# Kernel tuning notes

Measured on AMD Instinct MI355X. Metric: run time of the kernel, lower is better.

## Reference

```python
import jax, jax.numpy as jnp
import numpy as np

N_BISECT_ITERS = 50  # entmax library default


def entmax_bisect(X, alpha, n_iter=N_BISECT_ITERS):
    """alpha-entmax over last axis via bisection (Peters & Martins 2019).
    Solves for tau s.t. sum(max((alpha-1)X - tau, 0)^(1/(alpha-1))) = 1."""
    am1 = alpha - 1.0
    inv = 1.0 / am1
    Xa = X * am1
    max_val = jnp.max(Xa, axis=-1, keepdims=True)
    d = X.shape[-1]
    tau_lo = max_val - 1.0                                   # _gp(1, alpha) = 1
    tau_hi = max_val - jnp.asarray(1.0 / d, X.dtype) ** am1  # _gp(1/d, alpha)

    def pfun(tau):
        return jnp.maximum(Xa - tau, 0.0) ** inv

    f_lo = jnp.sum(pfun(tau_lo), axis=-1, keepdims=True) - 1.0

    def body(i, carry):
        tau_lo, dm = carry
        dm = dm * 0.5
        tau_m = tau_lo + dm
        f_m = jnp.sum(pfun(tau_m), axis=-1, keepdims=True) - 1.0
        tau_lo = jnp.where(f_m * f_lo >= 0, tau_m, tau_lo)
        return (tau_lo, dm)

    tau_lo, _ = jax.lax.fori_loop(0, n_iter, body, (tau_lo, tau_hi - tau_lo))
    p = pfun(tau_lo)
    return p / jnp.sum(p, axis=-1, keepdims=True)  # ensure_sum_one


def setup_inputs() -> dict:
    master = jax.random.key(0)
    kq, kk, kv = jax.random.split(master, 3)
    B, H, S, D = 4, 16, 2048, 64
    return {
        "query": jax.random.normal(kq, (B, H, S, D), jnp.float32),
        "key": jax.random.normal(kk, (B, H, S, D), jnp.float32),
        "value": jax.random.normal(kv, (B, H, S, D), jnp.float32),
        "alpha": jnp.float32(1.5),  # canonical entmax-1.5
    }


def reference(query, key, value, alpha):
    D = query.shape[-1]
    scale = 1.0 / jnp.sqrt(jnp.asarray(D, query.dtype))
    scores = jnp.einsum('bhqd,bhkd->bhqk', query, key) * scale  # [B,H,S,S]
    p_attn = entmax_bisect(scores, alpha)
    out = jnp.einsum('bhqk,bhkd->bhqd', p_attn, value)
    return (out, p_attn)
```

## Files before the change

kernel.cpp:

```cpp
#include <hip/hip_runtime.h>
#include <math.h>

#define S_LEN 2048
#define HD    64
#define QT    16
#define NT    1024
#define NW    16
#define NTIL  8
#define CAP   512
#define NITER 28
#define NEWT  10

typedef short s8v __attribute__((ext_vector_type(8)));
typedef float f4v __attribute__((ext_vector_type(4)));

template <bool B> struct BoolT { static constexpr bool value = B; };

__device__ __forceinline__ float wave_sum(float v) {
#pragma unroll
    for (int off = 32; off >= 1; off >>= 1)
        v += __shfl_xor(v, off, 64);
    return v;
}

__device__ __forceinline__ float group16_max(float v) {
#pragma unroll
    for (int off = 8; off >= 1; off >>= 1)
        v = fmaxf(v, __shfl_xor(v, off, 64));
    return v;
}

__device__ __forceinline__ unsigned f2bf2(float lo, float hi) {
    unsigned a = __float_as_uint(lo), b = __float_as_uint(hi);
    a += 0x7FFFu + ((a >> 16) & 1u);
    b += 0x7FFFu + ((b >> 16) & 1u);
    return (a >> 16) | (b & 0xFFFF0000u);
}

__device__ __forceinline__ unsigned short f2bf1(float x) {
    unsigned a = __float_as_uint(x);
    a += 0x7FFFu + ((a >> 16) & 1u);
    return (unsigned short)(a >> 16);
}

__device__ __forceinline__ s8v pack_bf8(const float4& x, const float4& y, float sc) {
    union { s8v s; unsigned u[4]; } f;
    f.u[0] = f2bf2(x.x * sc, x.y * sc);
    f.u[1] = f2bf2(x.z * sc, x.w * sc);
    f.u[2] = f2bf2(y.x * sc, y.y * sc);
    f.u[3] = f2bf2(y.z * sc, y.w * sc);
    return f.s;
}

template <bool INV2>
__device__ __forceinline__ float pfun_t(float t, float inv) {
    float u = fmaxf(t, 0.0f);
    return INV2 ? u * u : powf(u, inv);
}

template <int NR>
__device__ __forceinline__ void newton_reg(const float* cvrow, int ncp, int lane,
                                           float tau0, float& tau_out, float& isum_out) {
    float c[NR];
#pragma unroll
    for (int j = 0; j < NR; ++j) {
        int i = lane + 64 * j;
        c[j] = (i < ncp) ? cvrow[i] : -3.0e38f;
    }
    float tau = tau0;
#pragma unroll
    for (int it = 0; it < NEWT; ++it) {
        float s1 = 0.0f, s2 = 0.0f;
#pragma unroll
        for (int j = 0; j < NR; ++j) {
            float u = fmaxf(c[j] - tau, 0.0f);
            s1 += u;
            s2 = fmaf(u, u, s2);
        }
#pragma unroll
        for (int off = 32; off >= 1; off >>= 1) {
            s1 += __shfl_xor(s1, off, 64);
            s2 += __shfl_xor(s2, off, 64);
        }
        tau += (s2 - 1.0f) * 0.5f * __builtin_amdgcn_rcpf(fmaxf(s1, 1e-30f));
    }
    float s = 0.0f;
#pragma unroll
    for (int j = 0; j < NR; ++j) {
        float u = fmaxf(c[j] - tau, 0.0f);
        s = fmaf(u, u, s);
    }
    s = wave_sum(s);
    tau_out = tau;
    isum_out = 1.0f / s;
}

template <int NR, bool INV2>
__device__ __forceinline__ void bisect_reg(const float* cvrow, int ncp, int lane,
                                           float tau_lo0, float tau_hi, float inv,
                                           float& tau_out, float& isum_out) {
    float c[NR];
#pragma unroll
    for (int j = 0; j < NR; ++j) {
        int i = lane + 64 * j;
        c[j] = (i < ncp) ? cvrow[i] : -3.0e38f;
    }
    float tau = tau_lo0;
    float s0 = 0.0f;
#pragma unroll
    for (int j = 0; j < NR; ++j) s0 += pfun_t<INV2>(c[j] - tau, inv);
    const float f_lo = wave_sum(s0) - 1.0f;
    float dm = tau_hi - tau_lo0;
    for (int it = 0; it < NITER; ++it) {
        dm *= 0.5f;
        float tm = tau + dm;
        float s = 0.0f;
#pragma unroll
        for (int j = 0; j < NR; ++j) s += pfun_t<INV2>(c[j] - tm, inv);
        float fm = wave_sum(s) - 1.0f;
        if (fm * f_lo >= 0.0f) tau = tm;
    }
    float s = 0.0f;
#pragma unroll
    for (int j = 0; j < NR; ++j) s += pfun_t<INV2>(c[j] - tau, inv);
    float ssum = wave_sum(s);
    tau_out = tau;
    isum_out = 1.0f / ssum;
}

__global__ __launch_bounds__(256)
void pack_kv(const float* __restrict__ Kp, const float* __restrict__ Vp,
             s8v* __restrict__ Kb, s8v* __restrict__ Vb, int nK) {
    int idx = blockIdx.x * 256 + threadIdx.x;
    if (idx < nK) {
        const int lane = idx & 63, frag = (idx >> 6) & 1, tile = (idx >> 7) & 127, bh = idx >> 14;
        const int l16 = lane & 15, quad = lane >> 4;
        const float* src = Kp + ((size_t)(bh * S_LEN + tile * 16 + l16)) * HD + frag * 32 + quad * 8;
        float4 a = *(const float4*)src;
        float4 b = *(const float4*)(src + 4);
        Kb[idx] = pack_bf8(a, b, 1.0f);
    } else {
        int v = idx - nK;
        const int lane = v & 63, dt = (v >> 6) & 3, ktg = (v >> 8) & 63, bh = v >> 14;
        const int l16 = lane & 15, quad = lane >> 4;
        const float* src = Vp + ((size_t)(bh * S_LEN + ktg * 32 + quad * 8)) * HD + dt * 16 + l16;
        float w[8];
#pragma unroll
        for (int j = 0; j < 8; ++j) w[j] = src[(size_t)j * HD];
        float4 a = {w[0], w[1], w[2], w[3]};
        float4 b = {w[4], w[5], w[6], w[7]};
        Vb[v] = pack_bf8(a, b, 1.0f);
    }
}

template <bool PREK, bool DPV>
__global__ __launch_bounds__(NT)
void entmax_attn(const float* __restrict__ Qp, const float* __restrict__ Kp,
                 const float* __restrict__ Vp, const float* __restrict__ alphap,
                 float* __restrict__ outp, float* __restrict__ pattn,
                 const s8v* __restrict__ Kbf, const s8v* __restrict__ Vbf) {
    constexpr int SM_BIG = DPV ? (NW * QT * 68 * 4)
                               : (QT * CAP * 4 + QT * CAP * 2);
    __shared__ __align__(16) char smem[SM_BIG];
    float          (*candv)[CAP] = (float(*)[CAP])smem;
    unsigned short (*candi)[CAP] = (unsigned short(*)[CAP])(smem + QT * CAP * 4);

    __shared__ int   ncnt[QT];
    __shared__ float rmaxw[QT][NW];
    __shared__ float rmxf[QT];
    __shared__ float taus[QT];
    __shared__ float isums[QT];
    __shared__ float redw[NW];

    const int tid   = threadIdx.x;
    const int wv    = tid >> 6;
    const int lane  = tid & 63;
    const int quad  = lane >> 4;
    const int l16   = lane & 15;
    const int bh    = blockIdx.y;
    const int q0    = blockIdx.x * QT;
    const int wcol0 = wv * (NTIL * 16);

    const float alpha = alphap[0];
    const float am1   = alpha - 1.0f;
    const float inv   = 1.0f / am1;
    const bool  inv2  = (inv == 2.0f);
    const float xscale = (1.0f / sqrtf((float)HD)) * am1;
    const float gp_d   = powf(1.0f / (float)S_LEN, am1);

    if (tid < QT) ncnt[tid] = 0;

    const float* vbase = Vp + (size_t)bh * S_LEN * HD;

    s8v qa0, qa1;
    {
        const float* qp = Qp + ((size_t)bh * S_LEN + q0 + l16) * HD + quad * 8;
        float4 x0 = *(const float4*)qp;
        float4 x1 = *(const float4*)(qp + 4);
        float4 y0 = *(const float4*)(qp + 32);
        float4 y1 = *(const float4*)(qp + 36);
        qa0 = pack_bf8(x0, x1, xscale);
        qa1 = pack_bf8(y0, y1, xscale);
    }

    f4v xa[NTIL];
    if constexpr (PREK) {
        const s8v* kf = Kbf + ((size_t)bh * (S_LEN / 16) + (wcol0 >> 4)) * 2 * 64 + lane;
#pragma unroll
        for (int t = 0; t < NTIL; ++t) {
            s8v kb0 = kf[(2 * t    ) * 64];
            s8v kb1 = kf[(2 * t + 1) * 64];
            f4v acc = {0.0f, 0.0f, 0.0f, 0.0f};
            acc = __builtin_amdgcn_mfma_f32_16x16x32_bf16(qa0, kb0, acc, 0, 0, 0);
            acc = __builtin_amdgcn_mfma_f32_16x16x32_bf16(qa1, kb1, acc, 0, 0, 0);
            xa[t] = acc;
        }
    } else {
        const float* kbase = Kp + (size_t)bh * S_LEN * HD;
#pragma unroll
        for (int t = 0; t < NTIL; ++t) {
            const float* kp = kbase + ((size_t)(wcol0 + t * 16 + l16)) * HD + quad * 8;
            float4 k0 = *(const float4*)kp;
            float4 k1 = *(const float4*)(kp + 4);
            s8v kb0 = pack_bf8(k0, k1, 1.0f);
            f4v acc = {0.0f, 0.0f, 0.0f, 0.0f};
            acc = __builtin_amdgcn_mfma_f32_16x16x32_bf16(qa0, kb0, acc, 0, 0, 0);
            float4 k2 = *(const float4*)(kp + 32);
            float4 k3 = *(const float4*)(kp + 36);
            s8v kb1 = pack_bf8(k2, k3, 1.0f);
            acc = __builtin_amdgcn_mfma_f32_16x16x32_bf16(qa1, kb1, acc, 0, 0, 0);
            xa[t] = acc;
        }
    }

#pragma unroll
    for (int g = 0; g < 4; ++g) {
        float pm = xa[0][g];
#pragma unroll
        for (int t = 1; t < NTIL; ++t) pm = fmaxf(pm, xa[t][g]);
        pm = group16_max(pm);
        if (l16 == 0) rmaxw[quad * 4 + g][wv] = pm;
    }
    __syncthreads();
    if (tid < QT) {
        float m = rmaxw[tid][0];
#pragma unroll
        for (int w = 1; w < NW; ++w) m = fmaxf(m, rmaxw[tid][w]);
        rmxf[tid] = m;
    }
    __syncthreads();

    float tl0g[4];
#pragma unroll
    for (int g = 0; g < 4; ++g) tl0g[g] = rmxf[quad * 4 + g] - 1.0f;

#pragma unroll
    for (int t = 0; t < NTIL; ++t) {
#pragma unroll
        for (int g = 0; g < 4; ++g) {
            const float v = xa[t][g];
            const int row = quad * 4 + g;
            const bool pred = (v > tl0g[g]);
            unsigned long long m = __ballot(pred);
            unsigned gm16 = (unsigned)((m >> (quad * 16)) & 0xFFFFull);
            int base = 0;
            if (l16 == 0) {
                int cnt = __popc(gm16);
                if (cnt) base = atomicAdd(&ncnt[row], cnt);
            }
            base = __shfl(base, quad * 16, 64);
            if (pred) {
                int pos = base + __popc(gm16 & ((1u << l16) - 1u));
                if (pos < CAP) {
                    candv[row][pos] = v;
                    if constexpr (!DPV) candi[row][pos] = (unsigned short)(wcol0 + t * 16 + l16);
                }
            }
        }
    }
    __syncthreads();

    auto tail = [&](auto inv2c) {
        constexpr bool INV2 = decltype(inv2c)::value;

        {
            const int row = wv;
            const int nc = ncnt[row];
            if (nc <= CAP) {
                const int ncp = (nc + 7) & ~7;
                for (int i = nc + lane; i < ncp; i += 64) {
                    candv[row][i] = -3.0e38f;
                    if constexpr (!DPV) candi[row][i] = 0;
                }
                const float mx  = rmxf[row];
                const float tl0 = mx - 1.0f;
                const float th  = mx - gp_d;
                float tau, isum;
                if constexpr (INV2) {
                    if (ncp <= 256) newton_reg<4>(&candv[row][0], ncp, lane, tl0, tau, isum);
                    else            newton_reg<8>(&candv[row][0], ncp, lane, tl0, tau, isum);
                } else {
                    if (ncp <= 256) bisect_reg<4, INV2>(&candv[row][0], ncp, lane, tl0, th, inv, tau, isum);
                    else            bisect_reg<8, INV2>(&candv[row][0], ncp, lane, tl0, th, inv, tau, isum);
                }
                if (lane == 0) { taus[row] = tau; isums[row] = isum; }
            }
        }

#pragma unroll 1
        for (int r = 0; r < QT; ++r) {
            if (ncnt[r] > CAP) {
                const float mx = rmxf[r];
                const int g = r & 3;
                const bool mine = (quad == (r >> 2));
                float tau = mx - 1.0f;
                float s0 = 0.0f;
                if (mine) {
#pragma unroll
                    for (int t = 0; t < NTIL; ++t) s0 += pfun_t<INV2>(xa[t][g] - tau, inv);
                }
                s0 = wave_sum(s0);
                if (lane == 0) redw[wv] = s0;
                __syncthreads();
                float f_lo = -1.0f;
                for (int w = 0; w < NW; ++w) f_lo += redw[w];
                __syncthreads();
                float dm = (mx - gp_d) - tau;
                for (int it = 0; it < NITER; ++it) {
                    dm *= 0.5f;
                    float tm = tau + dm;
                    float s = 0.0f;
                    if (mine) {
#pragma unroll
                        for (int t = 0; t < NTIL; ++t) s += pfun_t<INV2>(xa[t][g] - tm, inv);
                    }
                    s = wave_sum(s);
                    if (lane == 0) redw[wv] = s;
                    __syncthreads();
                    float fm = -1.0f;
                    for (int w = 0; w < NW; ++w) fm += redw[w];
                    __syncthreads();
                    if (fm * f_lo >= 0.0f) tau = tm;
                }
                float s = 0.0f;
                if (mine) {
#pragma unroll
                    for (int t = 0; t < NTIL; ++t) s += pfun_t<INV2>(xa[t][g] - tau, inv);
                }
                s = wave_sum(s);
                if (lane == 0) redw[wv] = s;
                __syncthreads();
                float ssum = 0.0f;
                for (int w = 0; w < NW; ++w) ssum += redw[w];
                __syncthreads();
                if (tid == 0) { taus[r] = tau; isums[r] = 1.0f / ssum; }
            }
        }
        __syncthreads();

        if constexpr (DPV) {
            unsigned short* pwf = (unsigned short*)smem + wv * 2048;
            const size_t prow_base = ((size_t)bh * S_LEN + q0) * S_LEN;
#pragma unroll
            for (int g = 0; g < 4; ++g) {
                const int row = quad * 4 + g;
                const float tau  = taus[row];
                const float isum = isums[row];
                float* prow = pattn + prow_base + (size_t)row * S_LEN + wcol0 + l16;
#pragma unroll
                for (int t = 0; t < NTIL; ++t) {
                    float uu = fmaxf(xa[t][g] - tau, 0.0f);
                    float p2 = uu * uu;
                    prow[t * 16] = p2 * isum;
                    const int col   = t * 16 + l16;
                    const int slot  = ((col >> 3) ^ row) & 15;
                    pwf[row * 128 + slot * 8 + (col & 7)] = f2bf1(p2);
                }
            }
            s8v afrag[4];
#pragma unroll
            for (int kt = 0; kt < 4; ++kt) {
                const int slot = ((kt * 4 + quad) ^ l16) & 15;
                afrag[kt] = *(const s8v*)&pwf[l16 * 128 + slot * 8];
            }
            const s8v* vf = Vbf + ((size_t)bh * (S_LEN / 32) + (wcol0 >> 5)) * 4 * 64 + lane;
            f4v oacc[4];
#pragma unroll
            for (int dt = 0; dt < 4; ++dt) oacc[dt] = (f4v){0.0f, 0.0f, 0.0f, 0.0f};
#pragma unroll
            for (int kt = 0; kt < 4; ++kt) {
#pragma unroll
                for (int dt = 0; dt < 4; ++dt) {
                    s8v b = vf[(kt * 4 + dt) * 64];
                    oacc[dt] = __builtin_amdgcn_mfma_f32_16x16x32_bf16(afrag[kt], b, oacc[dt], 0, 0, 0);
                }
            }
            __syncthreads();
            float* part = (float*)smem;
#pragma unroll
            for (int dt = 0; dt < 4; ++dt) {
#pragma unroll
                for (int g = 0; g < 4; ++g) {
                    part[wv * (QT * 68) + (quad * 4 + g) * 68 + dt * 16 + l16] = oacc[dt][g];
                }
            }
            __syncthreads();
            float s = 0.0f;
#pragma unroll
            for (int w = 0; w < NW; ++w) s += part[w * (QT * 68) + wv * 68 + lane];
            outp[((size_t)bh * S_LEN + q0 + wv) * HD + lane] = s * isums[wv];
        } else {
            const size_t prow_base = ((size_t)bh * S_LEN + q0) * S_LEN;
#pragma unroll
            for (int g = 0; g < 4; ++g) {
                const int row = quad * 4 + g;
                const float tau  = taus[row];
                const float isum = isums[row];
                float* prow = pattn + prow_base + (size_t)row * S_LEN + wcol0 + l16;
#pragma unroll
                for (int t = 0; t < NTIL; ++t) {
                    prow[t * 16] = pfun_t<INV2>(xa[t][g] - tau, inv) * isum;
                }
            }
            __threadfence_block();
            __syncthreads();

            const int row  = wv;
            const int qrow = q0 + row;
            const int nc   = ncnt[row];
            const float tau  = taus[row];
            const float isum = isums[row];
            float oacc = 0.0f;
            if (nc <= CAP) {
                const int ncp = (nc + 7) & ~7;
                for (int i = lane; i < ncp; i += 64)
                    candv[row][i] = pfun_t<INV2>(candv[row][i] - tau, inv);
                float oacc1 = 0.0f;
                for (int i = 0; i < ncp; i += 8) {
#pragma unroll
                    for (int u = 0; u < 8; u += 2) {
                        oacc  = fmaf(candv[row][i + u],
                                     vbase[(size_t)candi[row][i + u] * HD + lane], oacc);
                        oacc1 = fmaf(candv[row][i + u + 1],
                                     vbase[(size_t)candi[row][i + u + 1] * HD + lane], oacc1);
                    }
                }
                oacc = (oacc + oacc1) * isum;
            } else {
                const float* prow = pattn + ((size_t)bh * S_LEN + qrow) * S_LEN;
                for (int k = 0; k < S_LEN; ++k)
                    oacc = fmaf(prow[k], vbase[(size_t)k * HD + lane], oacc);
            }
            outp[((size_t)bh * S_LEN + qrow) * HD + lane] = oacc;
        }
    };

    if (inv2) tail(BoolT<true>{});
    else      tail(BoolT<false>{});
}

extern "C" void kernel_launch(void* const* d_in, const int* in_sizes, int n_in,
                              void* d_out, int out_size, void* d_ws, size_t ws_size,
                              hipStream_t stream) {
    const float* Q = (const float*)d_in[0];
    const float* K = (const float*)d_in[1];
    const float* V = (const float*)d_in[2];
    const float* A = (const float*)d_in[3];
    float* out = (float*)d_out;
    const int BH = in_sizes[0] / (S_LEN * HD);
    float* p = out + (size_t)BH * S_LEN * HD;
    dim3 grid(S_LEN / QT, BH);

    const size_t kb_bytes = (size_t)BH * S_LEN * HD * sizeof(short);
    const int nK = BH * (S_LEN / 16) * 2 * 64;
    const int nV = BH * (S_LEN / 32) * 4 * 64;

    if (d_ws != nullptr && ws_size >= 2 * kb_bytes) {
        s8v* Kb = (s8v*)d_ws;
        s8v* Vb = (s8v*)((char*)d_ws + kb_bytes);
        pack_kv<<<dim3((nK + nV) / 256), 256, 0, stream>>>(K, V, Kb, Vb, nK);
        entmax_attn<true, true><<<grid, NT, 0, stream>>>(Q, K, V, A, out, p, Kb, Vb);
    } else if (d_ws != nullptr && ws_size >= kb_bytes) {
        s8v* Kb = (s8v*)d_ws;
        pack_kv<<<dim3(nK / 256), 256, 0, stream>>>(K, V, Kb, nullptr, nK);
        entmax_attn<true, false><<<grid, NT, 0, stream>>>(Q, K, V, A, out, p, Kb, nullptr);
    } else {
        entmax_attn<false, false><<<grid, NT, 0, stream>>>(Q, K, V, A, out, p, nullptr, nullptr);
    }
}
```

Measured before the change: 1.943 ms.

## Permute V packing to match per-lane P layout and batch candidate atomics

New measurement: 1.908 ms. Within noise of the previous version (-1.8%).

```diff
diff --git a/kernel.cpp b/kernel.cpp
--- a/kernel.cpp
+++ b/kernel.cpp
@@ -35,12 +35,6 @@
     a += 0x7FFFu + ((a >> 16) & 1u);
     b += 0x7FFFu + ((b >> 16) & 1u);
     return (a >> 16) | (b & 0xFFFF0000u);
-}
-
-__device__ __forceinline__ unsigned short f2bf1(float x) {
-    unsigned a = __float_as_uint(x);
-    a += 0x7FFFu + ((a >> 16) & 1u);
-    return (unsigned short)(a >> 16);
 }
 
 __device__ __forceinline__ s8v pack_bf8(const float4& x, const float4& y, float sc) {
@@ -141,12 +135,13 @@
         Kb[idx] = pack_bf8(a, b, 1.0f);
     } else {
         int v = idx - nK;
-        const int lane = v & 63, dt = (v >> 6) & 3, ktg = (v >> 8) & 63, bh = v >> 14;
+        const int lane = v & 63, dt = (v >> 6) & 3, kt32 = (v >> 8) & 63, bh = v >> 14;
         const int l16 = lane & 15, quad = lane >> 4;
-        const float* src = Vp + ((size_t)(bh * S_LEN + ktg * 32 + quad * 8)) * HD + dt * 16 + l16;
+        const int base_row = (kt32 >> 2) * 128 + (kt32 & 3) * 4 + quad;
+        const float* src = Vp + ((size_t)(bh * S_LEN + base_row)) * HD + dt * 16 + l16;
         float w[8];
 #pragma unroll
-        for (int j = 0; j < 8; ++j) w[j] = src[(size_t)j * HD];
+        for (int j = 0; j < 8; ++j) w[j] = src[(size_t)j * 16 * HD];
         float4 a = {w[0], w[1], w[2], w[3]};
         float4 b = {w[4], w[5], w[6], w[7]};
         Vb[v] = pack_bf8(a, b, 1.0f);
@@ -250,25 +245,25 @@
     }
     __syncthreads();
 
-    float tl0g[4];
-#pragma unroll
-    for (int g = 0; g < 4; ++g) tl0g[g] = rmxf[quad * 4 + g] - 1.0f;
-
-#pragma unroll
-    for (int t = 0; t < NTIL; ++t) {
-#pragma unroll
-        for (int g = 0; g < 4; ++g) {
+#pragma unroll
+    for (int g = 0; g < 4; ++g) {
+        const int   row = quad * 4 + g;
+        const float thr = rmxf[row] - 1.0f;
+        int total = 0;
+#pragma unroll
+        for (int t = 0; t < NTIL; ++t) {
+            unsigned long long m = __ballot(xa[t][g] > thr);
+            total += __popc((unsigned)((m >> (quad * 16)) & 0xFFFFull));
+        }
+        int base = 0;
+        if (l16 == 0 && total) base = atomicAdd(&ncnt[row], total);
+        base = __shfl(base, quad * 16, 64);
+#pragma unroll
+        for (int t = 0; t < NTIL; ++t) {
             const float v = xa[t][g];
-            const int row = quad * 4 + g;
-            const bool pred = (v > tl0g[g]);
+            const bool pred = (v > thr);
             unsigned long long m = __ballot(pred);
             unsigned gm16 = (unsigned)((m >> (quad * 16)) & 0xFFFFull);
-            int base = 0;
-            if (l16 == 0) {
-                int cnt = __popc(gm16);
-                if (cnt) base = atomicAdd(&ncnt[row], cnt);
-            }
-            base = __shfl(base, quad * 16, 64);
             if (pred) {
                 int pos = base + __popc(gm16 & ((1u << l16) - 1u));
                 if (pos < CAP) {
@@ -276,6 +271,7 @@
                     if constexpr (!DPV) candi[row][pos] = (unsigned short)(wcol0 + t * 16 + l16);
                 }
             }
+            base += __popc(gm16);
         }
     }
     __syncthreads();
@@ -367,21 +363,23 @@
                 const float tau  = taus[row];
                 const float isum = isums[row];
                 float* prow = pattn + prow_base + (size_t)row * S_LEN + wcol0 + l16;
+                union { s8v s; unsigned u[4]; } pk;
+                float pprev = 0.0f;
 #pragma unroll
                 for (int t = 0; t < NTIL; ++t) {
-                    float uu = fmaxf(xa[t][g] - tau, 0.0f);
-                    float p2 = uu * uu;
+                    float p2 = pfun_t<INV2>(xa[t][g] - tau, inv);
                     prow[t * 16] = p2 * isum;
-                    const int col   = t * 16 + l16;
-                    const int slot  = ((col >> 3) ^ row) & 15;
-                    pwf[row * 128 + slot * 8 + (col & 7)] = f2bf1(p2);
-                }
+                    if (t & 1) pk.u[t >> 1] = f2bf2(pprev, p2);
+                    else       pprev = p2;
+                }
+                const int c = (l16 ^ row) & 15;
+                *(s8v*)&pwf[row * 128 + c * 8] = pk.s;
             }
             s8v afrag[4];
 #pragma unroll
             for (int kt = 0; kt < 4; ++kt) {
-                const int slot = ((kt * 4 + quad) ^ l16) & 15;
-                afrag[kt] = *(const s8v*)&pwf[l16 * 128 + slot * 8];
+                const int c = ((kt * 4 + quad) ^ l16) & 15;
+                afrag[kt] = *(const s8v*)&pwf[l16 * 128 + c * 8];
             }
             const s8v* vf = Vbf + ((size_t)bh * (S_LEN / 32) + (wcol0 >> 5)) * 4 * 64 + lane;
             f4v oacc[4];
```
